# Optimization experiments

Measured on AMD Instinct MI355X. Metric: run time of the kernel, lower is better.

The kernel has to match this reference:

```python
import jax, jax.numpy as jnp
import numpy as np

N_CH = 62
F_DIM = 16
T_DIM = 32
B_DIM = 256
N_NODES = B_DIM * N_CH  # 15872
E_DIM = 200000
SEQ = T_DIM * F_DIM  # 512


def setup_inputs() -> dict:
    key = jax.random.key(0)
    ks = iter(jax.random.split(key, 40))
    s = 0.05
    inp = {}
    inp['x'] = jax.random.normal(next(ks), (N_NODES, F_DIM, T_DIM), dtype=jnp.float32)
    inp['edge_index'] = jax.random.randint(next(ks), (T_DIM, 2, E_DIM), 0, N_NODES, dtype=jnp.int64)
    inp['edge_weight'] = jax.random.uniform(next(ks), (T_DIM, E_DIM), dtype=jnp.float32)
    inp['batch'] = jax.random.randint(next(ks), (T_DIM, N_NODES), 0, B_DIM, dtype=jnp.int64)
    # ChebConv params (K=2): lins have no bias, single bias added at end
    for p in ['c1', 'c2']:
        inp[p + '_w0'] = jax.random.normal(next(ks), (F_DIM, F_DIM), dtype=jnp.float32) * s
        inp[p + '_w1'] = jax.random.normal(next(ks), (F_DIM, F_DIM), dtype=jnp.float32) * s
        inp[p + '_b'] = jnp.zeros((F_DIM,), jnp.float32)
    # LSTM params (torch gate order i,f,g,o); fold b_ih+b_hh into one bias
    for name, i_dim, h_dim in [('l1', N_CH, 64), ('l2', 64, 128), ('l3', 128, 256)]:
        inp[name + '_wih'] = jax.random.normal(next(ks), (4 * h_dim, i_dim), dtype=jnp.float32) * s
        inp[name + '_whh'] = jax.random.normal(next(ks), (4 * h_dim, h_dim), dtype=jnp.float32) * s
        inp[name + '_b'] = jnp.zeros((4 * h_dim,), jnp.float32)
    # MLP head
    for name, i_dim, o_dim in [('fc1', SEQ * 256, 256), ('fc2', 256, 128), ('fc3', 128, 64), ('fc4', 64, 4)]:
        inp[name + '_w'] = jax.random.normal(next(ks), (i_dim, o_dim), dtype=jnp.float32) * s
        inp[name + '_b'] = jnp.zeros((o_dim,), jnp.float32)
    return inp


def _cheb(x, src, dst, w, w0, w1, b):
    # PyG ChebConv K=2, sym norm, lambda_max=2: Tx1 = -D^{-1/2} A D^{-1/2} x
    n = x.shape[0]
    deg = jax.ops.segment_sum(w, src, num_segments=n)
    dinv = jnp.where(deg > 0, jax.lax.rsqrt(deg), 0.0)
    norm = -dinv[src] * w * dinv[dst]
    tx1 = jax.ops.segment_sum(norm[:, None] * x[src], dst, num_segments=n)
    return x @ w0 + tx1 @ w1 + b


def _lstm(x, wih, whh, b):
    # x: [B, S, I] -> [B, S, H], batch_first, zero init state
    bsz, _, _ = x.shape
    h_dim = whh.shape[1]
    xg = x @ wih.T + b  # precompute input gates [B, S, 4H]
    def step(carry, xt):
        h, c = carry
        g = xt + h @ whh.T
        i, f, gg, o = jnp.split(g, 4, axis=-1)
        c = jax.nn.sigmoid(f) * c + jax.nn.sigmoid(i) * jnp.tanh(gg)
        h = jax.nn.sigmoid(o) * jnp.tanh(c)
        return (h, c), h
    h0 = jnp.zeros((bsz, h_dim), x.dtype)
    _, hs = jax.lax.scan(step, (h0, h0), jnp.swapaxes(xg, 0, 1))
    return jnp.swapaxes(hs, 0, 1)


def reference(x, edge_index, edge_weight, batch,
              c1_w0, c1_w1, c1_b, c2_w0, c2_w1, c2_b,
              l1_wih, l1_whh, l1_b, l2_wih, l2_whh, l2_b, l3_wih, l3_whh, l3_b,
              fc1_w, fc1_b, fc2_w, fc2_b, fc3_w, fc3_b, fc4_w, fc4_b):
    def per_t(xt, ei, w):
        h = _cheb(xt, ei[0], ei[1], w, c1_w0, c1_w1, c1_b)
        h = jax.nn.leaky_relu(h, 0.01)
        return _cheb(h, ei[0], ei[1], w, c2_w0, c2_w1, c2_b)
    xt_first = jnp.moveaxis(x, -1, 0)  # [T, N, F]
    h = jax.vmap(per_t)(xt_first, edge_index, edge_weight)  # [T, N, F]
    xc = jnp.moveaxis(h, 0, -1)  # [N, F, T]
    xc = xc.reshape(B_DIM, N_CH, F_DIM, T_DIM)
    xc = jnp.transpose(xc, (0, 3, 2, 1))  # [B, T, F, 62]
    xc = xc.reshape(B_DIM, T_DIM * F_DIM, N_CH)  # [B, S, 62]
    h = _lstm(xc, l1_wih, l1_whh, l1_b)
    h = _lstm(h, l2_wih, l2_whh, l2_b)
    h = _lstm(h, l3_wih, l3_whh, l3_b)
    z = h.reshape(B_DIM, -1)  # [B, S*256]
    z = jax.nn.relu(z @ fc1_w + fc1_b)
    z = jax.nn.relu(z @ fc2_w + fc2_b)
    z = jax.nn.relu(z @ fc3_w + fc3_b)
    return z @ fc4_w + fc4_b
```

## Files before the change

kernel.cpp:

```cpp
#include <hip/hip_runtime.h>
#include <cstdint>
#include <cstddef>


#define T_DIM 32
#define F_DIMC 16
#define NNODE 15872
#define EDGES 200000
#define BATCH 256
#define SEQL 512
#define TN (T_DIM * NNODE)
#define TE (T_DIM * EDGES)

typedef unsigned short ushortT;
typedef __bf16 bf16_t;
typedef bf16_t bf16x8 __attribute__((ext_vector_type(8)));
typedef float f32x4 __attribute__((ext_vector_type(4)));

__device__ __forceinline__ ushortT f2bf(float f) {
  union { float f; unsigned u; } v; v.f = f;
  unsigned u = v.u;
  u += 0x7fffu + ((u >> 16) & 1u);
  return (ushortT)(u >> 16);
}
__device__ __forceinline__ float fsig(float x) { return 1.0f / (1.0f + __expf(-x)); }
__device__ __forceinline__ float ftanh(float x) {
  float e = __expf(2.0f * x);
  return 1.0f - 2.0f / (e + 1.0f);
}
#define PIN(v) asm volatile("" : "+v"(v))

__device__ __forceinline__ void bar_sync() {
  asm volatile("s_waitcnt lgkmcnt(0)\n\ts_barrier" ::: "memory");
  __builtin_amdgcn_sched_barrier(0);
}

__global__ void k_wprep(const float* __restrict__ w1i, const float* __restrict__ w1h,
                        const float* __restrict__ w2i, const float* __restrict__ w2h,
                        const float* __restrict__ w3i, const float* __restrict__ w3h,
                        ushortT* __restrict__ Wcat) {
  int id = blockIdx.x * 256 + threadIdx.x;
  if (id >= 524288) return;
  float v;
  if (id < 32768) {
    int g = id >> 7, k = id & 127;
    v = (k < 62) ? w1i[g * 62 + k] : ((k >= 64) ? w1h[g * 64 + (k - 64)] : 0.0f);
  } else if (id < 131072) {
    int j = id - 32768; int g = j / 192, k = j % 192;
    v = (k < 64) ? w2i[g * 64 + k] : w2h[g * 128 + (k - 64)];
  } else {
    int j = id - 131072; int g = j / 384, k = j % 384;
    v = (k < 128) ? w3i[g * 128 + k] : w3h[g * 256 + (k - 128)];
  }
  Wcat[id] = f2bf(v);
}

__global__ void k_transpose(const float* __restrict__ x, float* __restrict__ xt) {
  __shared__ float s[528];
  int n = blockIdx.x;
  int tid = threadIdx.x;
  for (int i = tid; i < 512; i += 256) {
    s[(i >> 5) * 33 + (i & 31)] = x[(size_t)n * 512 + i];
  }
  __syncthreads();
  for (int i = tid; i < 512; i += 256) {
    int t = i >> 4, f = i & 15;
    xt[((size_t)t * NNODE + n) * 16 + f] = s[f * 33 + t];
  }
}

__global__ void k_degcount(const int* __restrict__ ei, const float* __restrict__ ew,
                           float* __restrict__ deg, int* __restrict__ counts) {
  int id = blockIdx.x * 256 + threadIdx.x;
  if (id >= TE) return;
  int t = id / EDGES, e = id % EDGES;
  int src = ei[(2 * t) * EDGES + e];
  int dst = ei[(2 * t + 1) * EDGES + e];
  atomicAdd(&deg[t * NNODE + src], ew[id]);
  atomicAdd(&counts[t * NNODE + dst], 1);
}

__global__ void k_dinv(float* __restrict__ deg) {
  int id = blockIdx.x * 256 + threadIdx.x;
  if (id >= TN) return;
  float d = deg[id];
  deg[id] = (d > 0.0f) ? rsqrtf(d) : 0.0f;
}

__global__ void k_scanA(const int* __restrict__ counts, int* __restrict__ offs,
                        int* __restrict__ ctot) {
  __shared__ int s[256];
  int tid = threadIdx.x;
  int gid = blockIdx.x * 256 + tid;
  int v = counts[gid];
  s[tid] = v; __syncthreads();
  for (int off = 1; off < 256; off <<= 1) {
    int x = (tid >= off) ? s[tid - off] : 0;
    __syncthreads();
    s[tid] += x;
    __syncthreads();
  }
  offs[gid] = s[tid] - v;
  if (tid == 255) ctot[blockIdx.x] = s[255];
}

__global__ void k_scanB(const int* __restrict__ ctot, int* __restrict__ cbase) {
  __shared__ int s[256];
  int tid = threadIdx.x;
  int carry = 0;
  for (int c = 0; c < 8; ++c) {
    int i = c * 256 + tid;
    int v = (i < 1984) ? ctot[i] : 0;
    s[tid] = v; __syncthreads();
    for (int off = 1; off < 256; off <<= 1) {
      int x = (tid >= off) ? s[tid - off] : 0;
      __syncthreads();
      s[tid] += x;
      __syncthreads();
    }
    if (i < 1984) cbase[i] = carry + s[tid] - v;
    int tot = s[255];
    __syncthreads();
    carry += tot;
  }
}

__global__ void k_scanC(int* __restrict__ offs, const int* __restrict__ cbase) {
  int id = blockIdx.x * 256 + threadIdx.x;
  if (id >= TN) return;
  offs[id] += cbase[id >> 8];
}

__global__ void k_fill(const int* __restrict__ ei, const float* __restrict__ ew,
                       const float* __restrict__ dinv, const int* __restrict__ offs,
                       int* __restrict__ fillc, int* __restrict__ csrs,
                       float* __restrict__ csrn) {
  int id = blockIdx.x * 256 + threadIdx.x;
  if (id >= TE) return;
  int t = id / EDGES, e = id % EDGES;
  int src = ei[(2 * t) * EDGES + e];
  int dst = ei[(2 * t + 1) * EDGES + e];
  int idx = t * NNODE + dst;
  int pos = offs[idx] + atomicAdd(&fillc[idx], 1);
  csrs[pos] = src;
  csrn[pos] = -dinv[t * NNODE + src] * ew[id] * dinv[idx];
}

__device__ __forceinline__ void fma4(float4& a, float sc, const float4 b) {
  a.x += sc * b.x; a.y += sc * b.y; a.z += sc * b.z; a.w += sc * b.w;
}

__global__ void k_gc(const float* __restrict__ in, const int* __restrict__ offs,
                     const int* __restrict__ csrs, const float* __restrict__ csrn,
                     const float* __restrict__ w0, const float* __restrict__ w1,
                     const float* __restrict__ bias, float* __restrict__ outF,
                     ushortT* __restrict__ outX, int mode) {
  __shared__ float sw0[256], sw1[256], sb[16];
  int tid = threadIdx.x;
  sw0[tid] = w0[tid];
  sw1[tid] = w1[tid];
  if (tid < 16) sb[tid] = bias[tid];
  __syncthreads();
  int idx = blockIdx.x * 256 + tid;
  if (idx >= TN) return;
  int t = idx / NNODE, n = idx % NNODE;
  const float4* rowp = (const float4*)(in + (size_t)idx * 16);
  float4 x0 = rowp[0], x1 = rowp[1], x2 = rowp[2], x3 = rowp[3];
  float4 a0 = {0, 0, 0, 0}, a1 = {0, 0, 0, 0}, a2 = {0, 0, 0, 0}, a3 = {0, 0, 0, 0};
  int beg = offs[idx];
  int end = (idx == TN - 1) ? TE : offs[idx + 1];
  const float* base = in + (size_t)t * NNODE * 16;
  for (int p2 = beg; p2 < end; ++p2) {
    int s = csrs[p2];
    float nr = csrn[p2];
    const float4* rp = (const float4*)(base + (size_t)s * 16);
    fma4(a0, nr, rp[0]); fma4(a1, nr, rp[1]); fma4(a2, nr, rp[2]); fma4(a3, nr, rp[3]);
  }
  float xr[16], ar[16];
  *(float4*)&xr[0] = x0; *(float4*)&xr[4] = x1; *(float4*)&xr[8] = x2; *(float4*)&xr[12] = x3;
  *(float4*)&ar[0] = a0; *(float4*)&ar[4] = a1; *(float4*)&ar[8] = a2; *(float4*)&ar[12] = a3;
  float o[16];
#pragma unroll
  for (int j = 0; j < 16; ++j) o[j] = sb[j];
#pragma unroll
  for (int k = 0; k < 16; ++k) {
    float xv = xr[k], av = ar[k];
#pragma unroll
    for (int j = 0; j < 16; ++j) o[j] += xv * sw0[k * 16 + j] + av * sw1[k * 16 + j];
  }
  if (mode == 0) {
#pragma unroll
    for (int j = 0; j < 16; ++j) o[j] = (o[j] > 0.0f) ? o[j] : 0.01f * o[j];
    float4* op = (float4*)(outF + (size_t)idx * 16);
    op[0] = *(float4*)&o[0]; op[1] = *(float4*)&o[4];
    op[2] = *(float4*)&o[8]; op[3] = *(float4*)&o[12];
  } else {
    int bb = n / 62, ch = n % 62;
#pragma unroll
    for (int j = 0; j < 16; ++j)
      outX[((size_t)(bb * 512 + t * 16 + j)) * 64 + ch] = f2bf(o[j]);
  }
}

__global__ __launch_bounds__(512, 1) void k_lstm(const ushortT* __restrict__ xc,
                                                 const ushortT* __restrict__ Wcat,
                                                 const float* __restrict__ b1g,
                                                 const float* __restrict__ b2g,
                                                 const float* __restrict__ b3g,
                                                 ushortT* __restrict__ zbuf,
                                                 uint32_t* __restrict__ h2x,
                                                 uint32_t* __restrict__ xbuf) {
  __shared__ ushortT X1[2][16 * 72];
  __shared__ ushortT H1[2][16 * 72];
  __shared__ ushortT H2[2][16 * 136];
  __shared__ ushortT HS[2][16 * 136];
  __shared__ ushortT PS[2][16 * 136];
  __shared__ ushortT H2S[2][16 * 136];
  int tid = threadIdx.x;
  int wv = tid >> 6, lane = tid & 63;
  int col = lane & 15, koff = (lane >> 4) * 8, m = lane & 15;
  int bx = blockIdx.x;

  if (bx < 16) {
    int g = bx;
    int bg = g * 16;
    const ushortT* W1 = Wcat;
    const ushortT* W2 = Wcat + 32768;

    bf16x8 w1r[4][4];
    if (wv < 4) {
#pragma unroll
      for (int q = 0; q < 4; ++q)
#pragma unroll
        for (int k = 0; k < 4; ++k) {
          w1r[q][k] = *reinterpret_cast<const bf16x8*>(
              &W1[(size_t)(q * 64 + wv * 16 + col) * 128 + k * 32 + koff]);
          PIN(w1r[q][k]);
        }
    }
    bf16x8 w2r[4][6];
#pragma unroll
    for (int q = 0; q < 4; ++q)
#pragma unroll
      for (int k = 0; k < 6; ++k) {
        w2r[q][k] = *reinterpret_cast<const bf16x8*>(
            &W2[(size_t)(q * 128 + wv * 16 + col) * 192 + k * 32 + koff]);
        PIN(w2r[q][k]);
      }
    float b1v[4] = {0, 0, 0, 0}, b2v[4];
    if (wv < 4) {
#pragma unroll
      for (int q = 0; q < 4; ++q) b1v[q] = b1g[q * 64 + wv * 16 + col];
    }
#pragma unroll
    for (int q = 0; q < 4; ++q) b2v[q] = b2g[q * 128 + wv * 16 + col];

    float c1r[4] = {0, 0, 0, 0};
    float c2r[4] = {0, 0, 0, 0};

    for (int i = tid; i < 2 * 16 * 72; i += 512) { X1[0][i] = 0; H1[0][i] = 0; }
    for (int i = tid; i < 2 * 16 * 136; i += 512) H2[0][i] = 0;
    __syncthreads();
    uint4 xreg = {0, 0, 0, 0};
    {
      int tid2 = tid - 256;
      if (tid2 >= 0 && tid2 < 128) {
        int mm = tid2 >> 3, jj = (tid2 & 7) * 8;
        *(uint4*)&X1[0][mm * 72 + jj] =
            *(const uint4*)&xc[((size_t)(bg + mm) * 512 + 0) * 64 + jj];
        xreg = *(const uint4*)&xc[((size_t)(bg + mm) * 512 + 1) * 64 + jj];
      }
    }
    __syncthreads();

    uint32_t* h2g = h2x + (size_t)g * 512 * 2048;

    for (int t = 0; t < 512; ++t) {
      int pr = t & 1, pw = 1 - pr;
      if (wv < 4) {
        f32x4 acc[4] = {};
#pragma unroll
        for (int kt = 0; kt < 4; ++kt) {
          const ushortT* ap = (kt < 2) ? &X1[pr][m * 72 + kt * 32 + koff]
                                       : &H1[pr][m * 72 + (kt - 2) * 32 + koff];
          bf16x8 a = *reinterpret_cast<const bf16x8*>(ap);
#pragma unroll
          for (int q = 0; q < 4; ++q)
            acc[q] = __builtin_amdgcn_mfma_f32_16x16x32_bf16(a, w1r[q][kt], acc[q], 0, 0, 0);
        }
#pragma unroll
        for (int r = 0; r < 4; ++r) {
          int row = (lane >> 4) * 4 + r;
          int lc = wv * 16 + col;
          float gi = acc[0][r] + b1v[0];
          float gf = acc[1][r] + b1v[1];
          float gg = acc[2][r] + b1v[2];
          float go = acc[3][r] + b1v[3];
          float c = fsig(gf) * c1r[r] + fsig(gi) * ftanh(gg);
          float h = fsig(go) * ftanh(c);
          c1r[r] = c;
          H1[pw][row * 72 + lc] = f2bf(h);
        }
      } else {
        int tid2 = tid - 256;
        if (tid2 < 128) {
          int mm = tid2 >> 3, jj = (tid2 & 7) * 8;
          if (t + 1 < 512)
            *(uint4*)&X1[pw][mm * 72 + jj] = xreg;
          int tf = (t + 2 < 512) ? t + 2 : 511;
          xreg = *(const uint4*)&xc[((size_t)(bg + mm) * 512 + tf) * 64 + jj];
        }
      }
      bar_sync();
      {
        f32x4 acc[4] = {};
#pragma unroll
        for (int kt = 0; kt < 6; ++kt) {
          const ushortT* ap = (kt < 2) ? &H1[pw][m * 72 + kt * 32 + koff]
                                       : &H2[pr][m * 136 + (kt - 2) * 32 + koff];
          bf16x8 a = *reinterpret_cast<const bf16x8*>(ap);
#pragma unroll
          for (int q = 0; q < 4; ++q)
            acc[q] = __builtin_amdgcn_mfma_f32_16x16x32_bf16(a, w2r[q][kt], acc[q], 0, 0, 0);
        }
        uint32_t tag = ((uint32_t)(t + 1)) << 16;
#pragma unroll
        for (int r = 0; r < 4; ++r) {
          int row = (lane >> 4) * 4 + r;
          int lc = wv * 16 + col;
          float gi = acc[0][r] + b2v[0];
          float gf = acc[1][r] + b2v[1];
          float gg = acc[2][r] + b2v[2];
          float go = acc[3][r] + b2v[3];
          float c = fsig(gf) * c2r[r] + fsig(gi) * ftanh(gg);
          float h = fsig(go) * ftanh(c);
          c2r[r] = c;
          ushortT hb = f2bf(h);
          H2[pw][row * 136 + lc] = hb;
          __hip_atomic_store(&h2g[(size_t)t * 2048 + row * 128 + lc], tag | hb,
                             __ATOMIC_RELAXED, __HIP_MEMORY_SCOPE_AGENT);
        }
      }
      bar_sync();
    }
  } else {
    int bxx = bx - 16;
    int s = (bxx >> 3) & 1;
    int g = (bxx & 7) | ((bxx >> 4) << 3);
    int ps = 1 - s;
    int bg = g * 16;
    const ushortT* W3 = Wcat + 131072;

    bf16x8 wH[4][4], wO[4][4], wP[4][4];
#pragma unroll
    for (int q = 0; q < 4; ++q) {
      const ushortT* rw = &W3[(size_t)(q * 256 + s * 128 + wv * 16 + col) * 384];
#pragma unroll
      for (int j = 0; j < 4; ++j) {
        wH[q][j] = *reinterpret_cast<const bf16x8*>(&rw[j * 32 + koff]);
        wO[q][j] = *reinterpret_cast<const bf16x8*>(&rw[(4 + s * 4 + j) * 32 + koff]);
        wP[q][j] = *reinterpret_cast<const bf16x8*>(&rw[(4 + ps * 4 + j) * 32 + koff]);
        PIN(wH[q][j]); PIN(wO[q][j]); PIN(wP[q][j]);
      }
    }
    float b3v[4];
#pragma unroll
    for (int q = 0; q < 4; ++q) b3v[q] = b3g[q * 256 + s * 128 + wv * 16 + col];

    float c3r[4] = {0, 0, 0, 0};

    for (int i = tid; i < 2 * 16 * 136; i += 512) HS[0][i] = 0;
    __syncthreads();

    uint32_t* myslot = xbuf + (((size_t)g * 2 + s) * 2) * 2048;
    const uint32_t* pslot = xbuf + (((size_t)g * 2 + ps) * 2) * 2048;
    const uint32_t* h2g = h2x + (size_t)g * 512 * 2048;

    int prow = tid >> 5, pc0 = (tid & 31) * 4;

    {
      const uint32_t* hp = h2g + prow * 128 + pc0;
      uint32_t u0 = __hip_atomic_load(hp + 0, __ATOMIC_RELAXED, __HIP_MEMORY_SCOPE_AGENT);
      uint32_t u1 = __hip_atomic_load(hp + 1, __ATOMIC_RELAXED, __HIP_MEMORY_SCOPE_AGENT);
      uint32_t u2 = __hip_atomic_load(hp + 2, __ATOMIC_RELAXED, __HIP_MEMORY_SCOPE_AGENT);
      uint32_t u3 = __hip_atomic_load(hp + 3, __ATOMIC_RELAXED, __HIP_MEMORY_SCOPE_AGENT);
      for (;;) {
        bool ok = ((u0 >> 16) == 1u) & ((u1 >> 16) == 1u) &
                  ((u2 >> 16) == 1u) & ((u3 >> 16) == 1u);
        if (ok) break;
        u0 = __hip_atomic_load(hp + 0, __ATOMIC_RELAXED, __HIP_MEMORY_SCOPE_AGENT);
        u1 = __hip_atomic_load(hp + 1, __ATOMIC_RELAXED, __HIP_MEMORY_SCOPE_AGENT);
        u2 = __hip_atomic_load(hp + 2, __ATOMIC_RELAXED, __HIP_MEMORY_SCOPE_AGENT);
        u3 = __hip_atomic_load(hp + 3, __ATOMIC_RELAXED, __HIP_MEMORY_SCOPE_AGENT);
      }
      H2S[0][prow * 136 + pc0 + 0] = (ushortT)(u0 & 0xffffu);
      H2S[0][prow * 136 + pc0 + 1] = (ushortT)(u1 & 0xffffu);
      H2S[0][prow * 136 + pc0 + 2] = (ushortT)(u2 & 0xffffu);
      H2S[0][prow * 136 + pc0 + 3] = (ushortT)(u3 & 0xffffu);
    }
    __syncthreads();

    for (int t = 0; t < 512; ++t) {
      int prt = t & 1, pw = 1 - prt;
      const uint32_t* pb = pslot + (size_t)prt * 2048 + prow * 128 + pc0;
      uint32_t v0 = 0, v1 = 0, v2 = 0, v3 = 0;
      if (t > 0) {
        v0 = __hip_atomic_load(pb + 0, __ATOMIC_RELAXED, __HIP_MEMORY_SCOPE_AGENT);
        v1 = __hip_atomic_load(pb + 1, __ATOMIC_RELAXED, __HIP_MEMORY_SCOPE_AGENT);
        v2 = __hip_atomic_load(pb + 2, __ATOMIC_RELAXED, __HIP_MEMORY_SCOPE_AGENT);
        v3 = __hip_atomic_load(pb + 3, __ATOMIC_RELAXED, __HIP_MEMORY_SCOPE_AGENT);
      }
      const uint32_t* hp = h2g + (size_t)(t + 1) * 2048 + prow * 128 + pc0;
      uint32_t u0 = 0, u1 = 0, u2 = 0, u3 = 0;
      if (t < 511) {
        u0 = __hip_atomic_load(hp + 0, __ATOMIC_RELAXED, __HIP_MEMORY_SCOPE_AGENT);
        u1 = __hip_atomic_load(hp + 1, __ATOMIC_RELAXED, __HIP_MEMORY_SCOPE_AGENT);
        u2 = __hip_atomic_load(hp + 2, __ATOMIC_RELAXED, __HIP_MEMORY_SCOPE_AGENT);
        u3 = __hip_atomic_load(hp + 3, __ATOMIC_RELAXED, __HIP_MEMORY_SCOPE_AGENT);
      }
      __builtin_amdgcn_sched_barrier(0);
      f32x4 acc[4] = {};
#pragma unroll
      for (int kt = 0; kt < 4; ++kt) {
        bf16x8 a = *reinterpret_cast<const bf16x8*>(&H2S[prt][m * 136 + kt * 32 + koff]);
#pragma unroll
        for (int q = 0; q < 4; ++q)
          acc[q] = __builtin_amdgcn_mfma_f32_16x16x32_bf16(a, wH[q][kt], acc[q], 0, 0, 0);
      }
      if (t > 0) {
#pragma unroll
        for (int j = 0; j < 4; ++j) {
          bf16x8 a = *reinterpret_cast<const bf16x8*>(&HS[prt][m * 136 + j * 32 + koff]);
#pragma unroll
          for (int q = 0; q < 4; ++q)
            acc[q] = __builtin_amdgcn_mfma_f32_16x16x32_bf16(a, wO[q][j], acc[q], 0, 0, 0);
        }
        {
          uint32_t want = (uint32_t)t;
          while (((v0 >> 16) != want) | ((v1 >> 16) != want) |
                 ((v2 >> 16) != want) | ((v3 >> 16) != want)) {
            v0 = __hip_atomic_load(pb + 0, __ATOMIC_RELAXED, __HIP_MEMORY_SCOPE_AGENT);
            v1 = __hip_atomic_load(pb + 1, __ATOMIC_RELAXED, __HIP_MEMORY_SCOPE_AGENT);
            v2 = __hip_atomic_load(pb + 2, __ATOMIC_RELAXED, __HIP_MEMORY_SCOPE_AGENT);
            v3 = __hip_atomic_load(pb + 3, __ATOMIC_RELAXED, __HIP_MEMORY_SCOPE_AGENT);
          }
          PS[prt][prow * 136 + pc0 + 0] = (ushortT)(v0 & 0xffffu);
          PS[prt][prow * 136 + pc0 + 1] = (ushortT)(v1 & 0xffffu);
          PS[prt][prow * 136 + pc0 + 2] = (ushortT)(v2 & 0xffffu);
          PS[prt][prow * 136 + pc0 + 3] = (ushortT)(v3 & 0xffffu);
        }
        bar_sync();
#pragma unroll
        for (int j = 0; j < 4; ++j) {
          bf16x8 a = *reinterpret_cast<const bf16x8*>(&PS[prt][m * 136 + j * 32 + koff]);
#pragma unroll
          for (int q = 0; q < 4; ++q)
            acc[q] = __builtin_amdgcn_mfma_f32_16x16x32_bf16(a, wP[q][j], acc[q], 0, 0, 0);
        }
      }
      if (t < 511) {
        uint32_t want = (uint32_t)(t + 2);
        while (((u0 >> 16) != want) | ((u1 >> 16) != want) |
               ((u2 >> 16) != want) | ((u3 >> 16) != want)) {
          u0 = __hip_atomic_load(hp + 0, __ATOMIC_RELAXED, __HIP_MEMORY_SCOPE_AGENT);
          u1 = __hip_atomic_load(hp + 1, __ATOMIC_RELAXED, __HIP_MEMORY_SCOPE_AGENT);
          u2 = __hip_atomic_load(hp + 2, __ATOMIC_RELAXED, __HIP_MEMORY_SCOPE_AGENT);
          u3 = __hip_atomic_load(hp + 3, __ATOMIC_RELAXED, __HIP_MEMORY_SCOPE_AGENT);
        }
        H2S[pw][prow * 136 + pc0 + 0] = (ushortT)(u0 & 0xffffu);
        H2S[pw][prow * 136 + pc0 + 1] = (ushortT)(u1 & 0xffffu);
        H2S[pw][prow * 136 + pc0 + 2] = (ushortT)(u2 & 0xffffu);
        H2S[pw][prow * 136 + pc0 + 3] = (ushortT)(u3 & 0xffffu);
      }
      uint32_t* mw = myslot + (size_t)((t + 1) & 1) * 2048;
      ushortT hbs[4];
#pragma unroll
      for (int r = 0; r < 4; ++r) {
        int row = (lane >> 4) * 4 + r;
        int lc = wv * 16 + col;
        float gi = acc[0][r] + b3v[0];
        float gf = acc[1][r] + b3v[1];
        float gg = acc[2][r] + b3v[2];
        float go = acc[3][r] + b3v[3];
        float c = fsig(gf) * c3r[r] + fsig(gi) * ftanh(gg);
        float h = fsig(go) * ftanh(c);
        c3r[r] = c;
        hbs[r] = f2bf(h);
        __hip_atomic_store(mw + row * 128 + lc, ((uint32_t)(t + 1) << 16) | hbs[r],
                           __ATOMIC_RELAXED, __HIP_MEMORY_SCOPE_AGENT);
      }
      asm volatile("s_waitcnt vmcnt(0)" ::: "memory");
      __builtin_amdgcn_sched_barrier(0);
#pragma unroll
      for (int r = 0; r < 4; ++r) {
        int row = (lane >> 4) * 4 + r;
        int lc = wv * 16 + col;
        HS[pw][row * 136 + lc] = hbs[r];
        zbuf[((size_t)(bg + row) * 512 + t) * 256 + s * 128 + lc] = hbs[r];
      }
      bar_sync();
    }
  }
}

__global__ __launch_bounds__(256) void k_fc1(const ushortT* __restrict__ zbuf,
                                             const float* __restrict__ w,
                                             float* __restrict__ part) {
  __shared__ ushortT As[256 * 40];
  __shared__ ushortT Bs[64 * 40];
  int tid = threadIdx.x;
  int kb = blockIdx.x;
  int nb = blockIdx.y;
  int wv = tid >> 6, lane = tid & 63;
  int col = lane & 15, koff = (lane >> 4) * 8;
  int k0base = kb * 2048;
  f32x4 acc[4][4] = {};
  for (int kt = 0; kt < 64; ++kt) {
    int k0 = k0base + kt * 32;
    {
      const uint4* src = (const uint4*)(zbuf + (size_t)tid * 131072 + k0);
      uint4* dst = (uint4*)(As + tid * 40);
      dst[0] = src[0]; dst[1] = src[1]; dst[2] = src[2]; dst[3] = src[3];
    }
    {
      int kk = tid >> 3, j0 = (tid & 7) * 8;
      const float* srcw = w + (size_t)(k0 + kk) * 256 + nb * 64 + j0;
#pragma unroll
      for (int jj = 0; jj < 8; ++jj) Bs[(j0 + jj) * 40 + kk] = f2bf(srcw[jj]);
    }
    __syncthreads();
    bf16x8 bfr[4];
#pragma unroll
    for (int nt = 0; nt < 4; ++nt)
      bfr[nt] = *reinterpret_cast<const bf16x8*>(&Bs[(nt * 16 + col) * 40 + koff]);
#pragma unroll
    for (int mt = 0; mt < 4; ++mt) {
      bf16x8 afr = *reinterpret_cast<const bf16x8*>(&As[(wv * 64 + mt * 16 + col) * 40 + koff]);
#pragma unroll
      for (int nt = 0; nt < 4; ++nt)
        acc[mt][nt] = __builtin_amdgcn_mfma_f32_16x16x32_bf16(afr, bfr[nt], acc[mt][nt], 0, 0, 0);
    }
    __syncthreads();
  }
#pragma unroll
  for (int mt = 0; mt < 4; ++mt)
#pragma unroll
    for (int nt = 0; nt < 4; ++nt)
#pragma unroll
      for (int r = 0; r < 4; ++r) {
        int m = wv * 64 + mt * 16 + (lane >> 4) * 4 + r;
        int n = nb * 64 + nt * 16 + col;
        part[(size_t)kb * 65536 + m * 256 + n] = acc[mt][nt][r];
      }
}

__global__ void k_fc1red(const float* __restrict__ part, const float* __restrict__ b,
                         float* __restrict__ out) {
  int id = blockIdx.x * 256 + threadIdx.x;
  if (id >= 65536) return;
  float s = 0.0f;
  for (int kb = 0; kb < 64; ++kb) s += part[(size_t)kb * 65536 + id];
  s += b[id & 255];
  out[id] = fmaxf(s, 0.0f);
}

__global__ void k_fcv(const float* __restrict__ in, const float* __restrict__ w,
                      const float* __restrict__ b, float* __restrict__ out,
                      int K, int Nn, int doRelu) {
  int id = blockIdx.x * 256 + threadIdx.x;
  int m = id / Nn, n = id % Nn;
  float s = b[n];
  for (int k = 0; k < K; ++k) s += in[m * K + k] * w[k * Nn + n];
  if (doRelu) s = fmaxf(s, 0.0f);
  out[id] = s;
}

extern "C" void kernel_launch(void* const* d_in, const int* in_sizes, int n_in,
                              void* d_out, int out_size, void* d_ws, size_t ws_size,
                              hipStream_t stream) {
  (void)in_sizes; (void)n_in; (void)out_size; (void)ws_size;
  const float* x    = (const float*)d_in[0];
  const int* ei     = (const int*)d_in[1];
  const float* ew   = (const float*)d_in[2];
  const float* c1w0 = (const float*)d_in[4];
  const float* c1w1 = (const float*)d_in[5];
  const float* c1b  = (const float*)d_in[6];
  const float* c2w0 = (const float*)d_in[7];
  const float* c2w1 = (const float*)d_in[8];
  const float* c2b  = (const float*)d_in[9];
  const float* l1wi = (const float*)d_in[10];
  const float* l1wh = (const float*)d_in[11];
  const float* l1b  = (const float*)d_in[12];
  const float* l2wi = (const float*)d_in[13];
  const float* l2wh = (const float*)d_in[14];
  const float* l2b  = (const float*)d_in[15];
  const float* l3wi = (const float*)d_in[16];
  const float* l3wh = (const float*)d_in[17];
  const float* l3b  = (const float*)d_in[18];
  const float* fc1w = (const float*)d_in[19];
  const float* fc1b = (const float*)d_in[20];
  const float* fc2w = (const float*)d_in[21];
  const float* fc2b = (const float*)d_in[22];
  const float* fc3w = (const float*)d_in[23];
  const float* fc3b = (const float*)d_in[24];
  const float* fc4w = (const float*)d_in[25];
  const float* fc4b = (const float*)d_in[26];
  float* out = (float*)d_out;

  char* p = (char*)d_ws;
  auto alloc = [&](size_t bytes) { void* r = (void*)p; p += (bytes + 255) & ~(size_t)255; return r; };
  float* xt      = (float*)alloc(32505856);
  float* h1buf   = (float*)alloc(32505856);
  float* dinv    = (float*)alloc(2031616);
  int* counts    = (int*)alloc(2031616);
  int* offs      = (int*)alloc(2031616);
  int* fillc     = (int*)alloc(2031616);
  int* ctot      = (int*)alloc(8192);
  int* cbase     = (int*)alloc(8192);
  int* csrs      = (int*)alloc(25600000);
  float* csrn    = (float*)alloc(25600000);
  ushortT* xc    = (ushortT*)alloc(16777216);
  ushortT* Wcat  = (ushortT*)alloc(1048576);
  ushortT* zbuf  = (ushortT*)alloc(67108864);
  float* part    = (float*)alloc(16777216);
  float* fo1     = (float*)alloc(262144);
  float* fo2     = (float*)alloc(131072);
  float* fo3     = (float*)alloc(65536);
  uint32_t* xbuf = (uint32_t*)alloc(524288);
  uint32_t* h2x = (uint32_t*)xt;

  hipMemsetAsync(dinv, 0, 2031616, stream);
  hipMemsetAsync(counts, 0, 2031616, stream);
  hipMemsetAsync(fillc, 0, 2031616, stream);
  hipMemsetAsync(xc, 0, 16777216, stream);

  k_wprep<<<2048, 256, 0, stream>>>(l1wi, l1wh, l2wi, l2wh, l3wi, l3wh, Wcat);
  k_transpose<<<15872, 256, 0, stream>>>(x, xt);
  k_degcount<<<25000, 256, 0, stream>>>(ei, ew, dinv, counts);
  k_dinv<<<1984, 256, 0, stream>>>(dinv);
  k_scanA<<<1984, 256, 0, stream>>>(counts, offs, ctot);
  k_scanB<<<1, 256, 0, stream>>>(ctot, cbase);
  k_scanC<<<1984, 256, 0, stream>>>(offs, cbase);
  k_fill<<<25000, 256, 0, stream>>>(ei, ew, dinv, offs, fillc, csrs, csrn);
  k_gc<<<1984, 256, 0, stream>>>(xt, offs, csrs, csrn, c1w0, c1w1, c1b, h1buf, nullptr, 0);
  k_gc<<<1984, 256, 0, stream>>>(h1buf, offs, csrs, csrn, c2w0, c2w1, c2b, nullptr, xc, 1);
  hipMemsetAsync(h2x, 0, 67108864, stream);
  k_lstm<<<48, 512, 0, stream>>>(xc, Wcat, l1b, l2b, l3b, zbuf, h2x, xbuf);
  k_fc1<<<dim3(64, 4), 256, 0, stream>>>(zbuf, fc1w, part);
  k_fc1red<<<256, 256, 0, stream>>>(part, fc1b, fo1);
  k_fcv<<<128, 256, 0, stream>>>(fo1, fc2w, fc2b, fo2, 256, 128, 1);
  k_fcv<<<64, 256, 0, stream>>>(fo2, fc3w, fc3b, fo3, 128, 64, 1);
  k_fcv<<<4, 256, 0, stream>>>(fo3, fc4w, fc4b, out, 64, 4, 0);
}
```

Measured before the change: 3.614 ms.

## Process two batch groups per layer-3 LSTM block to halve layer-3 block count

```diff
diff --git a/kernel.cpp b/kernel.cpp
--- a/kernel.cpp
+++ b/kernel.cpp
@@ -213,9 +213,8 @@
   __shared__ ushortT X1[2][16 * 72];
   __shared__ ushortT H1[2][16 * 72];
   __shared__ ushortT H2[2][16 * 136];
-  __shared__ ushortT HS[2][16 * 136];
-  __shared__ ushortT PS[2][16 * 136];
-  __shared__ ushortT H2S[2][16 * 136];
+  __shared__ ushortT HSa[2][16 * 136], PSa[2][16 * 136], H2Sa[2][16 * 136];
+  __shared__ ushortT HSb[2][16 * 136], PSb[2][16 * 136], H2Sb[2][16 * 136];
   int tid = threadIdx.x;
   int wv = tid >> 6, lane = tid & 63;
   int col = lane & 15, koff = (lane >> 4) * 8, m = lane & 15;
@@ -344,11 +343,11 @@
       bar_sync();
     }
   } else {
-    int bxx = bx - 16;
-    int s = (bxx >> 3) & 1;
-    int g = (bxx & 7) | ((bxx >> 4) << 3);
+    int i = bx - 16;
+    int s = i >> 3;
+    int pi = i & 7;
     int ps = 1 - s;
-    int bg = g * 16;
+    int gA = 2 * pi, gB = 2 * pi + 1;
     const ushortT* W3 = Wcat + 131072;
 
     bf16x8 wH[4][4], wO[4][4], wP[4][4];
@@ -367,18 +366,25 @@
 #pragma unroll
     for (int q = 0; q < 4; ++q) b3v[q] = b3g[q * 256 + s * 128 + wv * 16 + col];
 
-    float c3r[4] = {0, 0, 0, 0};
-
-    for (int i = tid; i < 2 * 16 * 136; i += 512) HS[0][i] = 0;
-    __syncthreads();
-
-    uint32_t* myslot = xbuf + (((size_t)g * 2 + s) * 2) * 2048;
-    const uint32_t* pslot = xbuf + (((size_t)g * 2 + ps) * 2) * 2048;
-    const uint32_t* h2g = h2x + (size_t)g * 512 * 2048;
+    float c3rA[4] = {0, 0, 0, 0};
+    float c3rB[4] = {0, 0, 0, 0};
+
+    for (int i2 = tid; i2 < 2 * 16 * 136; i2 += 512) { HSa[0][i2] = 0; HSb[0][i2] = 0; }
+    __syncthreads();
+
+    uint32_t* mslA = xbuf + (((size_t)gA * 2 + s) * 2) * 2048;
+    const uint32_t* pslA = xbuf + (((size_t)gA * 2 + ps) * 2) * 2048;
+    uint32_t* mslB = xbuf + (((size_t)gB * 2 + s) * 2) * 2048;
+    const uint32_t* pslB = xbuf + (((size_t)gB * 2 + ps) * 2) * 2048;
+    const uint32_t* h2gA = h2x + (size_t)gA * 512 * 2048;
+    const uint32_t* h2gB = h2x + (size_t)gB * 512 * 2048;
 
     int prow = tid >> 5, pc0 = (tid & 31) * 4;
 
-    {
+#pragma unroll
+    for (int grp = 0; grp < 2; ++grp) {
+      const uint32_t* h2g = grp ? h2gB : h2gA;
+      ushortT (&H2S)[2][16 * 136] = grp ? H2Sb : H2Sa;
       const uint32_t* hp = h2g + prow * 128 + pc0;
       uint32_t u0 = __hip_atomic_load(hp + 0, __ATOMIC_RELAXED, __HIP_MEMORY_SCOPE_AGENT);
       uint32_t u1 = __hip_atomic_load(hp + 1, __ATOMIC_RELAXED, __HIP_MEMORY_SCOPE_AGENT);
@@ -401,104 +407,116 @@
     __syncthreads();
 
     for (int t = 0; t < 512; ++t) {
-      int prt = t & 1, pw = 1 - prt;
-      const uint32_t* pb = pslot + (size_t)prt * 2048 + prow * 128 + pc0;
-      uint32_t v0 = 0, v1 = 0, v2 = 0, v3 = 0;
-      if (t > 0) {
-        v0 = __hip_atomic_load(pb + 0, __ATOMIC_RELAXED, __HIP_MEMORY_SCOPE_AGENT);
-        v1 = __hip_atomic_load(pb + 1, __ATOMIC_RELAXED, __HIP_MEMORY_SCOPE_AGENT);
-        v2 = __hip_atomic_load(pb + 2, __ATOMIC_RELAXED, __HIP_MEMORY_SCOPE_AGENT);
-        v3 = __hip_atomic_load(pb + 3, __ATOMIC_RELAXED, __HIP_MEMORY_SCOPE_AGENT);
-      }
-      const uint32_t* hp = h2g + (size_t)(t + 1) * 2048 + prow * 128 + pc0;
-      uint32_t u0 = 0, u1 = 0, u2 = 0, u3 = 0;
-      if (t < 511) {
-        u0 = __hip_atomic_load(hp + 0, __ATOMIC_RELAXED, __HIP_MEMORY_SCOPE_AGENT);
-        u1 = __hip_atomic_load(hp + 1, __ATOMIC_RELAXED, __HIP_MEMORY_SCOPE_AGENT);
-        u2 = __hip_atomic_load(hp + 2, __ATOMIC_RELAXED, __HIP_MEMORY_SCOPE_AGENT);
-        u3 = __hip_atomic_load(hp + 3, __ATOMIC_RELAXED, __HIP_MEMORY_SCOPE_AGENT);
-      }
-      __builtin_amdgcn_sched_barrier(0);
-      f32x4 acc[4] = {};
-#pragma unroll
-      for (int kt = 0; kt < 4; ++kt) {
-        bf16x8 a = *reinterpret_cast<const bf16x8*>(&H2S[prt][m * 136 + kt * 32 + koff]);
-#pragma unroll
-        for (int q = 0; q < 4; ++q)
-          acc[q] = __builtin_amdgcn_mfma_f32_16x16x32_bf16(a, wH[q][kt], acc[q], 0, 0, 0);
-      }
-      if (t > 0) {
-#pragma unroll
-        for (int j = 0; j < 4; ++j) {
-          bf16x8 a = *reinterpret_cast<const bf16x8*>(&HS[prt][m * 136 + j * 32 + koff]);
-#pragma unroll
-          for (int q = 0; q < 4; ++q)
-            acc[q] = __builtin_amdgcn_mfma_f32_16x16x32_bf16(a, wO[q][j], acc[q], 0, 0, 0);
-        }
-        {
-          uint32_t want = (uint32_t)t;
-          while (((v0 >> 16) != want) | ((v1 >> 16) != want) |
-                 ((v2 >> 16) != want) | ((v3 >> 16) != want)) {
-            v0 = __hip_atomic_load(pb + 0, __ATOMIC_RELAXED, __HIP_MEMORY_SCOPE_AGENT);
-            v1 = __hip_atomic_load(pb + 1, __ATOMIC_RELAXED, __HIP_MEMORY_SCOPE_AGENT);
-            v2 = __hip_atomic_load(pb + 2, __ATOMIC_RELAXED, __HIP_MEMORY_SCOPE_AGENT);
-            v3 = __hip_atomic_load(pb + 3, __ATOMIC_RELAXED, __HIP_MEMORY_SCOPE_AGENT);
-          }
-          PS[prt][prow * 136 + pc0 + 0] = (ushortT)(v0 & 0xffffu);
-          PS[prt][prow * 136 + pc0 + 1] = (ushortT)(v1 & 0xffffu);
-          PS[prt][prow * 136 + pc0 + 2] = (ushortT)(v2 & 0xffffu);
-          PS[prt][prow * 136 + pc0 + 3] = (ushortT)(v3 & 0xffffu);
-        }
-        bar_sync();
-#pragma unroll
-        for (int j = 0; j < 4; ++j) {
-          bf16x8 a = *reinterpret_cast<const bf16x8*>(&PS[prt][m * 136 + j * 32 + koff]);
-#pragma unroll
-          for (int q = 0; q < 4; ++q)
-            acc[q] = __builtin_amdgcn_mfma_f32_16x16x32_bf16(a, wP[q][j], acc[q], 0, 0, 0);
-        }
-      }
-      if (t < 511) {
-        uint32_t want = (uint32_t)(t + 2);
-        while (((u0 >> 16) != want) | ((u1 >> 16) != want) |
-               ((u2 >> 16) != want) | ((u3 >> 16) != want)) {
+      int prt = t & 1, pwt = 1 - prt;
+#pragma unroll
+      for (int grp = 0; grp < 2; ++grp) {
+        ushortT (&HS)[2][16 * 136]  = grp ? HSb : HSa;
+        ushortT (&PS)[2][16 * 136]  = grp ? PSb : PSa;
+        ushortT (&H2S)[2][16 * 136] = grp ? H2Sb : H2Sa;
+        float (&c3r)[4] = grp ? c3rB : c3rA;
+        uint32_t* myslot = grp ? mslB : mslA;
+        const uint32_t* pslot = grp ? pslB : pslA;
+        const uint32_t* h2g = grp ? h2gB : h2gA;
+        int bg = (grp ? gB : gA) * 16;
+
+        const uint32_t* pb = pslot + (size_t)prt * 2048 + prow * 128 + pc0;
+        uint32_t v0 = 0, v1 = 0, v2 = 0, v3 = 0;
+        if (t > 0) {
+          v0 = __hip_atomic_load(pb + 0, __ATOMIC_RELAXED, __HIP_MEMORY_SCOPE_AGENT);
+          v1 = __hip_atomic_load(pb + 1, __ATOMIC_RELAXED, __HIP_MEMORY_SCOPE_AGENT);
+          v2 = __hip_atomic_load(pb + 2, __ATOMIC_RELAXED, __HIP_MEMORY_SCOPE_AGENT);
+          v3 = __hip_atomic_load(pb + 3, __ATOMIC_RELAXED, __HIP_MEMORY_SCOPE_AGENT);
+        }
+        const uint32_t* hp = h2g + (size_t)(t + 1) * 2048 + prow * 128 + pc0;
+        uint32_t u0 = 0, u1 = 0, u2 = 0, u3 = 0;
+        if (t < 511) {
           u0 = __hip_atomic_load(hp + 0, __ATOMIC_RELAXED, __HIP_MEMORY_SCOPE_AGENT);
           u1 = __hip_atomic_load(hp + 1, __ATOMIC_RELAXED, __HIP_MEMORY_SCOPE_AGENT);
           u2 = __hip_atomic_load(hp + 2, __ATOMIC_RELAXED, __HIP_MEMORY_SCOPE_AGENT);
           u3 = __hip_atomic_load(hp + 3, __ATOMIC_RELAXED, __HIP_MEMORY_SCOPE_AGENT);
         }
-        H2S[pw][prow * 136 + pc0 + 0] = (ushortT)(u0 & 0xffffu);
-        H2S[pw][prow * 136 + pc0 + 1] = (ushortT)(u1 & 0xffffu);
-        H2S[pw][prow * 136 + pc0 + 2] = (ushortT)(u2 & 0xffffu);
-        H2S[pw][prow * 136 + pc0 + 3] = (ushortT)(u3 & 0xffffu);
-      }
-      uint32_t* mw = myslot + (size_t)((t + 1) & 1) * 2048;
-      ushortT hbs[4];
-#pragma unroll
-      for (int r = 0; r < 4; ++r) {
-        int row = (lane >> 4) * 4 + r;
-        int lc = wv * 16 + col;
-        float gi = acc[0][r] + b3v[0];
-        float gf = acc[1][r] + b3v[1];
-        float gg = acc[2][r] + b3v[2];
-        float go = acc[3][r] + b3v[3];
-        float c = fsig(gf) * c3r[r] + fsig(gi) * ftanh(gg);
-        float h = fsig(go) * ftanh(c);
-        c3r[r] = c;
-        hbs[r] = f2bf(h);
-        __hip_atomic_store(mw + row * 128 + lc, ((uint32_t)(t + 1) << 16) | hbs[r],
-                           __ATOMIC_RELAXED, __HIP_MEMORY_SCOPE_AGENT);
-      }
-      asm volatile("s_waitcnt vmcnt(0)" ::: "memory");
-      __builtin_amdgcn_sched_barrier(0);
-#pragma unroll
-      for (int r = 0; r < 4; ++r) {
-        int row = (lane >> 4) * 4 + r;
-        int lc = wv * 16 + col;
-        HS[pw][row * 136 + lc] = hbs[r];
-        zbuf[((size_t)(bg + row) * 512 + t) * 256 + s * 128 + lc] = hbs[r];
-      }
-      bar_sync();
+        __builtin_amdgcn_sched_barrier(0);
+        f32x4 acc[4] = {};
+#pragma unroll
+        for (int kt = 0; kt < 4; ++kt) {
+          bf16x8 a = *reinterpret_cast<const bf16x8*>(&H2S[prt][m * 136 + kt * 32 + koff]);
+#pragma unroll
+          for (int q = 0; q < 4; ++q)
+            acc[q] = __builtin_amdgcn_mfma_f32_16x16x32_bf16(a, wH[q][kt], acc[q], 0, 0, 0);
+        }
+        if (t > 0) {
+#pragma unroll
+          for (int j = 0; j < 4; ++j) {
+            bf16x8 a = *reinterpret_cast<const bf16x8*>(&HS[prt][m * 136 + j * 32 + koff]);
+#pragma unroll
+            for (int q = 0; q < 4; ++q)
+              acc[q] = __builtin_amdgcn_mfma_f32_16x16x32_bf16(a, wO[q][j], acc[q], 0, 0, 0);
+          }
+          {
+            uint32_t want = (uint32_t)t;
+            while (((v0 >> 16) != want) | ((v1 >> 16) != want) |
+                   ((v2 >> 16) != want) | ((v3 >> 16) != want)) {
+              v0 = __hip_atomic_load(pb + 0, __ATOMIC_RELAXED, __HIP_MEMORY_SCOPE_AGENT);
+              v1 = __hip_atomic_load(pb + 1, __ATOMIC_RELAXED, __HIP_MEMORY_SCOPE_AGENT);
+              v2 = __hip_atomic_load(pb + 2, __ATOMIC_RELAXED, __HIP_MEMORY_SCOPE_AGENT);
+              v3 = __hip_atomic_load(pb + 3, __ATOMIC_RELAXED, __HIP_MEMORY_SCOPE_AGENT);
+            }
+            PS[prt][prow * 136 + pc0 + 0] = (ushortT)(v0 & 0xffffu);
+            PS[prt][prow * 136 + pc0 + 1] = (ushortT)(v1 & 0xffffu);
+            PS[prt][prow * 136 + pc0 + 2] = (ushortT)(v2 & 0xffffu);
+            PS[prt][prow * 136 + pc0 + 3] = (ushortT)(v3 & 0xffffu);
+          }
+          bar_sync();
+#pragma unroll
+          for (int j = 0; j < 4; ++j) {
+            bf16x8 a = *reinterpret_cast<const bf16x8*>(&PS[prt][m * 136 + j * 32 + koff]);
+#pragma unroll
+            for (int q = 0; q < 4; ++q)
+              acc[q] = __builtin_amdgcn_mfma_f32_16x16x32_bf16(a, wP[q][j], acc[q], 0, 0, 0);
+          }
+        }
+        if (t < 511) {
+          uint32_t want = (uint32_t)(t + 2);
+          while (((u0 >> 16) != want) | ((u1 >> 16) != want) |
+                 ((u2 >> 16) != want) | ((u3 >> 16) != want)) {
+            u0 = __hip_atomic_load(hp + 0, __ATOMIC_RELAXED, __HIP_MEMORY_SCOPE_AGENT);
+            u1 = __hip_atomic_load(hp + 1, __ATOMIC_RELAXED, __HIP_MEMORY_SCOPE_AGENT);
+            u2 = __hip_atomic_load(hp + 2, __ATOMIC_RELAXED, __HIP_MEMORY_SCOPE_AGENT);
+            u3 = __hip_atomic_load(hp + 3, __ATOMIC_RELAXED, __HIP_MEMORY_SCOPE_AGENT);
+          }
+          H2S[pwt][prow * 136 + pc0 + 0] = (ushortT)(u0 & 0xffffu);
+          H2S[pwt][prow * 136 + pc0 + 1] = (ushortT)(u1 & 0xffffu);
+          H2S[pwt][prow * 136 + pc0 + 2] = (ushortT)(u2 & 0xffffu);
+          H2S[pwt][prow * 136 + pc0 + 3] = (ushortT)(u3 & 0xffffu);
+        }
+        uint32_t* mw = myslot + (size_t)((t + 1) & 1) * 2048;
+        ushortT hbs[4];
+#pragma unroll
+        for (int r = 0; r < 4; ++r) {
+          int row = (lane >> 4) * 4 + r;
+          int lc = wv * 16 + col;
+          float gi = acc[0][r] + b3v[0];
+          float gf = acc[1][r] + b3v[1];
+          float gg = acc[2][r] + b3v[2];
+          float go = acc[3][r] + b3v[3];
+          float c = fsig(gf) * c3r[r] + fsig(gi) * ftanh(gg);
+          float h = fsig(go) * ftanh(c);
+          c3r[r] = c;
+          hbs[r] = f2bf(h);
+          __hip_atomic_store(mw + row * 128 + lc, ((uint32_t)(t + 1) << 16) | hbs[r],
+                             __ATOMIC_RELAXED, __HIP_MEMORY_SCOPE_AGENT);
+        }
+        asm volatile("s_waitcnt vmcnt(0)" ::: "memory");
+        __builtin_amdgcn_sched_barrier(0);
+#pragma unroll
+        for (int r = 0; r < 4; ++r) {
+          int row = (lane >> 4) * 4 + r;
+          int lc = wv * 16 + col;
+          HS[pwt][row * 136 + lc] = hbs[r];
+          zbuf[((size_t)(bg + row) * 512 + t) * 256 + s * 128 + lc] = hbs[r];
+        }
+        bar_sync();
+      }
     }
   }
 }
@@ -645,7 +663,7 @@
   k_gc<<<1984, 256, 0, stream>>>(xt, offs, csrs, csrn, c1w0, c1w1, c1b, h1buf, nullptr, 0);
   k_gc<<<1984, 256, 0, stream>>>(h1buf, offs, csrs, csrn, c2w0, c2w1, c2b, nullptr, xc, 1);
   hipMemsetAsync(h2x, 0, 67108864, stream);
-  k_lstm<<<48, 512, 0, stream>>>(xc, Wcat, l1b, l2b, l3b, zbuf, h2x, xbuf);
+  k_lstm<<<32, 512, 0, stream>>>(xc, Wcat, l1b, l2b, l3b, zbuf, h2x, xbuf);
   k_fc1<<<dim3(64, 4), 256, 0, stream>>>(zbuf, fc1w, part);
   k_fc1red<<<256, 256, 0, stream>>>(part, fc1b, fo1);
   k_fcv<<<128, 256, 0, stream>>>(fo1, fc2w, fc2b, fo2, 256, 128, 1);
```

After: 6.099 ms. +68.8%, slower.
